# Kernel tuning notes

Measured on AMD Instinct MI355X. Metric: run time of the kernel, lower is better.

## Reference

```python
import jax, jax.numpy as jnp
import numpy as np

HEIGHT = 32
NEG = -1e30
K = 2
DEPTH_LIM = 3
BN_EPS = 1e-5


def blockwise_knn(x, k, depth_lim):
    # x: [B, C, N]. Returns global neighbor indices [B, N, k*width].
    B, C, N = x.shape
    width = N // HEIGHT
    k_eff = k * width
    xb = x.reshape(B, C, HEIGHT, width)
    win = 2 * depth_lim + 1
    offs = jnp.arange(win) - depth_lim

    def per_block(i):
        wb = i + offs
        valid = (wb >= 0) & (wb < HEIGHT)
        wbc = jnp.clip(wb, 0, HEIGHT - 1)
        cand = xb[:, :, wbc, :].reshape(B, C, win * width)   # [B,C,W]
        q = xb[:, :, i, :]                                   # [B,C,width]
        # negative squared distance: 2 q.c - |q|^2 - |c|^2 (topk largest = nearest)
        d = 2.0 * jnp.einsum('bcq,bcw->bqw', q, cand)
        d = d - jnp.sum(q * q, axis=1)[:, :, None] - jnp.sum(cand * cand, axis=1)[:, None, :]
        mask = jnp.repeat(valid, width)                      # [W]
        d = jnp.where(mask[None, None, :], d, NEG)
        _, loc = jax.lax.top_k(d, k_eff)                     # [B,width,k_eff]
        # window starts at block (i-depth_lim): local -> global point index
        return loc + (i - depth_lim) * width

    idx = jax.vmap(per_block, out_axes=1)(jnp.arange(HEIGHT))  # [B,32,width,k_eff]
    return idx.reshape(B, N, k_eff)


def get_graph_feature(x, k, depth_lim):
    B, C, N = x.shape
    idx = blockwise_knn(x, k, depth_lim)              # [B,N,K] int32
    xt = jnp.transpose(x, (0, 2, 1))                  # [B,N,C]
    feat = jax.vmap(lambda xb, ib: xb[ib])(xt, idx)   # [B,N,K,C] gather
    center = xt[:, :, None, :]
    f = jnp.concatenate([feat - center, jnp.broadcast_to(center, feat.shape)], axis=-1)
    return jnp.transpose(f, (0, 3, 1, 2))             # [B,2C,N,K]


def edge_layer(x, w, g, b, k, depth_lim):
    f = get_graph_feature(x, k, depth_lim)            # [B,2C,N,K]
    y = jnp.einsum('oc,bcnk->bonk', w, f)             # 1x1 conv, no bias
    # BatchNorm2d, train-mode batch statistics (biased variance)
    mu = jnp.mean(y, axis=(0, 2, 3), keepdims=True)
    var = jnp.mean((y - mu) ** 2, axis=(0, 2, 3), keepdims=True)
    y = (y - mu) / jnp.sqrt(var + BN_EPS) * g[None, :, None, None] + b[None, :, None, None]
    y = jnp.where(y >= 0, y, 0.2 * y)                 # LeakyReLU(0.2)
    return jnp.max(y, axis=-1)                        # max over neighbors -> [B,O,N]


def setup_inputs() -> dict:
    key = jax.random.key(0)
    ks = jax.random.split(key, 16)
    d = {}
    d['x'] = jax.random.normal(ks[0], (2, 256, 1024), jnp.float32)
    shapes = {'w0': (128, 512), 'w1': (128, 256), 'w2': (64, 256), 'w3': (64, 128)}
    for i, (name, sh) in enumerate(shapes.items()):
        d[name] = jax.random.normal(ks[1 + i], sh, jnp.float32) * (1.0 / np.sqrt(sh[1]))
        co = sh[0]
        d['g' + name[1]] = jax.random.uniform(ks[5 + i], (co,), jnp.float32, 0.5, 1.5)
        d['b' + name[1]] = jax.random.normal(ks[9 + i], (co,), jnp.float32) * 0.1
    d['w_last'] = jax.random.normal(ks[13], (384, 384), jnp.float32) * (1.0 / np.sqrt(384))
    return d


def reference(x, w0, g0, b0, w1, g1, b1, w2, g2, b2, w3, g3, b3, w_last):
    x0 = edge_layer(x, w0, g0, b0, K, DEPTH_LIM)          # [B,128,N]
    xnew = edge_layer(x0, w1, g1, b1, K, DEPTH_LIM)       # [B,128,N]
    xcon = jnp.concatenate([x0, xnew], axis=1)            # [B,256,N]
    xnew = edge_layer(xnew, w2, g2, b2, K, DEPTH_LIM)     # [B,64,N]
    xcon = jnp.concatenate([xcon, xnew], axis=1)          # [B,320,N]
    xnew = edge_layer(xnew, w3, g3, b3, K, DEPTH_LIM)     # [B,64,N]
    xcon = jnp.concatenate([xcon, xnew], axis=1)          # [B,384,N]
    return jnp.einsum('oc,bcn->bon', w_last, xcon)        # Conv1d k=1, no bias
```

## Files before the change

### kernel.cpp

```cpp
#include <hip/hip_runtime.h>
#include <math.h>

#define NPTS 1024
#define CAND 224
#define KEFF 64
#define BATCH 2
#define NEGV -1e30f
#define PLANE (BATCH * NPTS * CAND)

__global__ __launch_bounds__(256) void kprep(const float* __restrict__ w0, const float* __restrict__ w1,
                                             const float* __restrict__ w2, const float* __restrict__ w3,
                                             const float* __restrict__ wl, float* __restrict__ wt) {
    __shared__ float tA[32][33];
    __shared__ float tB[32][33];
    int id = blockIdx.x;
    int t = threadIdx.x;
    int row = t >> 5, col = t & 31;
    const float* W = w0; int Cin = 256, Co = 128; float* WtA = wt; float* WtB = wt + 32768;
    int tc = 0, to = 0; bool isWL = false;
    if (id < 32)      { int r = id;      tc = r >> 2; to = r & 3; }
    else if (id < 48) { W = w1; Cin = 128; Co = 128; WtA = wt + 65536;  WtB = wt + 81920;  int r = id - 32; tc = r >> 2; to = r & 3; }
    else if (id < 56) { W = w2; Cin = 128; Co = 64;  WtA = wt + 98304;  WtB = wt + 106496; int r = id - 48; tc = r >> 1; to = r & 1; }
    else if (id < 60) { W = w3; Cin = 64;  Co = 64;  WtA = wt + 114688; WtB = wt + 118784; int r = id - 56; tc = r >> 1; to = r & 1; }
    else { isWL = true; int r = id - 60; tc = r / 12; to = r % 12; }
    if (!isWL) {
#pragma unroll
        for (int r = 0; r < 4; ++r) {
            int o = to * 32 + row + r * 8;
            int c = tc * 32 + col;
            float va = W[(size_t)o * 2 * Cin + c];
            tA[row + r * 8][col] = va;
            tB[row + r * 8][col] = W[(size_t)o * 2 * Cin + Cin + c] - va;
        }
        __syncthreads();
#pragma unroll
        for (int r = 0; r < 4; ++r) {
            int c = tc * 32 + row + r * 8;
            int o = to * 32 + col;
            WtA[(size_t)c * Co + o] = tA[col][row + r * 8];
            WtB[(size_t)c * Co + o] = tB[col][row + r * 8];
        }
    } else {
        float* wlT = wt + 122880;
#pragma unroll
        for (int r = 0; r < 4; ++r) {
            int o = to * 32 + row + r * 8;
            int c = tc * 32 + col;
            tA[row + r * 8][col] = wl[(size_t)o * 384 + c];
        }
        __syncthreads();
#pragma unroll
        for (int r = 0; r < 4; ++r) {
            int c = tc * 32 + row + r * 8;
            int o = to * 32 + col;
            wlT[(size_t)c * 384 + o] = tA[col][row + r * 8];
        }
    }
}

struct GP {
    const float* xin; int bstride; int Cin; int Co; int nch; int applyBN;
    const float* WtA; const float* WtB;
    const float* partPrev; const float* gPrev; const float* bePrev;
    float* A; float* Bv; float* sq; float* Dp;
};

__global__ __launch_bounds__(256) void kgemm(GP p) {
    __shared__ float smem[7168];
    __shared__ float shsc[128];
    __shared__ float shsh[128];
    int t = threadIdx.x;
    if (p.applyBN && t < p.Cin) {
        const float* pp = p.partPrev;
        float s  = pp[t * 2]     + pp[(p.Cin + t) * 2];
        float s2 = pp[t * 2 + 1] + pp[(p.Cin + t) * 2 + 1];
        const float invc = 1.f / 131072.f;
        float mu = s * invc;
        float var = s2 * invc - mu * mu;
        float rs = rsqrtf(var + 1e-5f);
        float sc = p.gPrev[t] * rs;
        shsc[t] = sc;
        shsh[t] = p.bePrev[t] - mu * sc;
    }
    __syncthreads();
    int nOT = p.Co >> 6;
    int nABx = 32 * nOT * BATCH;
    if ((int)blockIdx.x < nABx) {
        int id = blockIdx.x;
        int nt = id & 31; int rest = id >> 5;
        int ot = rest % nOT; int b = rest / nOT;
        int tn2 = (t & 15) * 2, to4 = (t >> 4) * 4;
        int n0 = nt * 32, o0 = ot * 64;
        const float* xb = p.xin + (size_t)b * p.bstride + n0;
        float* Xs = smem; float* Wta = smem + 1024; float* Wtb = smem + 3200;
        float2 a2[4], b2[4], s2v;
#pragma unroll
        for (int i = 0; i < 4; ++i) { a2[i] = make_float2(0.f,0.f); b2[i] = make_float2(0.f,0.f); }
        s2v = make_float2(0.f,0.f);
        int xcc0 = t >> 5, xnn = t & 31;
        int wcc0 = t >> 6, woo = t & 63;
        for (int c0 = 0; c0 < p.Cin; c0 += 32) {
            float rx[4], ra[8], rb[8];
#pragma unroll
            for (int k = 0; k < 4; ++k)
                rx[k] = xb[(size_t)(c0 + xcc0 + k * 8) * NPTS + xnn];
#pragma unroll
            for (int k = 0; k < 8; ++k) {
                ra[k] = p.WtA[(size_t)(c0 + wcc0 + k * 4) * p.Co + o0 + woo];
                rb[k] = p.WtB[(size_t)(c0 + wcc0 + k * 4) * p.Co + o0 + woo];
            }
            if (p.applyBN) {
#pragma unroll
                for (int k = 0; k < 4; ++k) {
                    int cc = xcc0 + k * 8;
                    float y = fmaf(rx[k], shsc[c0 + cc], shsh[c0 + cc]);
                    rx[k] = y >= 0.f ? y : 0.2f * y;
                }
            }
            __syncthreads();
#pragma unroll
            for (int k = 0; k < 4; ++k)
                Xs[(xcc0 + k * 8) * 32 + xnn] = rx[k];
#pragma unroll
            for (int k = 0; k < 8; ++k) {
                Wta[(wcc0 + k * 4) * 68 + woo] = ra[k];
                Wtb[(wcc0 + k * 4) * 68 + woo] = rb[k];
            }
            __syncthreads();
#pragma unroll 8
            for (int cc = 0; cc < 32; ++cc) {
                float2 xv = *(const float2*)&Xs[cc * 32 + tn2];
                float4 wa = *(const float4*)&Wta[cc * 68 + to4];
                float4 wb = *(const float4*)&Wtb[cc * 68 + to4];
                s2v.x = fmaf(xv.x, xv.x, s2v.x);
                s2v.y = fmaf(xv.y, xv.y, s2v.y);
                float wav[4] = {wa.x, wa.y, wa.z, wa.w};
                float wbv[4] = {wb.x, wb.y, wb.z, wb.w};
#pragma unroll
                for (int i = 0; i < 4; ++i) {
                    a2[i].x = fmaf(wav[i], xv.x, a2[i].x);
                    a2[i].y = fmaf(wav[i], xv.y, a2[i].y);
                    b2[i].x = fmaf(wbv[i], xv.x, b2[i].x);
                    b2[i].y = fmaf(wbv[i], xv.y, b2[i].y);
                }
            }
        }
        int n = n0 + tn2;
        if (ot == 0 && to4 == 0)
            *(float2*)&p.sq[b * NPTS + n] = s2v;
#pragma unroll
        for (int i = 0; i < 4; ++i) {
            int o = o0 + to4 + i;
            size_t off = ((size_t)(b * p.Co + o)) * NPTS + n;
            *(float2*)&p.A[off] = a2[i];
            *(float2*)&p.Bv[off] = b2[i];
        }
    } else {
        int id2 = blockIdx.x - nABx;
        int chunk = id2 % p.nch; int rest = id2 / p.nch;
        int i = rest & 31; int b = rest >> 5;
        int c0 = chunk * 32;
        const float* xb = p.xin + (size_t)b * p.bstride;
        float* Xc = smem;
        int q = t >> 3;
        int wg = t & 7;
        float r[28];
        int rcc[28], rw[28];
#pragma unroll
        for (int k = 0; k < 28; ++k) {
            int e = t + k * 256;
            int cc = e / CAND;
            int w  = e - cc * CAND;
            rcc[k] = cc; rw[k] = w;
            int wb = i - 3 + (w >> 5);
            wb = wb < 0 ? 0 : (wb > 31 ? 31 : wb);
            r[k] = xb[(size_t)(c0 + cc) * NPTS + wb * 32 + (w & 31)];
        }
        if (p.applyBN) {
#pragma unroll
            for (int k = 0; k < 28; ++k) {
                float y = fmaf(r[k], shsc[c0 + rcc[k]], shsh[c0 + rcc[k]]);
                r[k] = y >= 0.f ? y : 0.2f * y;
            }
        }
#pragma unroll
        for (int k = 0; k < 28; ++k)
            Xc[rcc[k] * CAND + rw[k]] = r[k];
        __syncthreads();
        float acc[28];
#pragma unroll
        for (int j = 0; j < 28; ++j) acc[j] = 0.f;
        for (int cc = 0; cc < 32; ++cc) {
            float qv = Xc[cc * CAND + 96 + q];
            const float4* row = (const float4*)&Xc[cc * CAND + wg * 28];
#pragma unroll
            for (int j4 = 0; j4 < 7; ++j4) {
                float4 v = row[j4];
                acc[j4 * 4 + 0] = fmaf(qv, v.x, acc[j4 * 4 + 0]);
                acc[j4 * 4 + 1] = fmaf(qv, v.y, acc[j4 * 4 + 1]);
                acc[j4 * 4 + 2] = fmaf(qv, v.z, acc[j4 * 4 + 2]);
                acc[j4 * 4 + 3] = fmaf(qv, v.w, acc[j4 * 4 + 3]);
            }
        }
        int n = i * 32 + q;
        size_t base = (((size_t)chunk * BATCH + b) * NPTS + n) * CAND + wg * 28;
        float4* outp = (float4*)&p.Dp[base];
#pragma unroll
        for (int j4 = 0; j4 < 7; ++j4)
            outp[j4] = make_float4(acc[j4 * 4], acc[j4 * 4 + 1], acc[j4 * 4 + 2], acc[j4 * 4 + 3]);
    }
}

template<int NCH>
__global__ __launch_bounds__(256) void kselect(const float* __restrict__ Dp,
                                               const float* __restrict__ sq,
                                               int* __restrict__ idxo) {
    __shared__ ulonglong2 Dsh2[4][112];
    unsigned long long* Dsh = (unsigned long long*)Dsh2;
    int t = threadIdx.x;
    int wv = t >> 6, l = t & 63;
    int b = blockIdx.y;
    int n = blockIdx.x * 4 + wv;
    int i = n >> 5;
    float sqn = sq[b * NPTS + n];
    float pr[4][NCH];
    float sqw[4];
#pragma unroll
    for (int j = 0; j < 4; ++j) {
        int w = l + 64 * j;
        if (w < CAND) {
            size_t off = ((size_t)b * NPTS + n) * CAND + w;
#pragma unroll
            for (int ch = 0; ch < NCH; ++ch)
                pr[j][ch] = Dp[off + (size_t)ch * PLANE];
            int wb = i - 3 + (w >> 5);
            int wbc = wb < 0 ? 0 : (wb > 31 ? 31 : wb);
            sqw[j] = sq[b * NPTS + wbc * 32 + (w & 31)];
        }
    }
    unsigned long long kj[4];
#pragma unroll
    for (int j = 0; j < 4; ++j) {
        int w = l + 64 * j;
        if (w < CAND) {
            float s = 0.f;
#pragma unroll
            for (int ch = 0; ch < NCH; ++ch) s += pr[j][ch];
            int wb = i - 3 + (w >> 5);
            bool valid = (wb >= 0) && (wb < 32);
            float d = 2.f * s - sqn - sqw[j];
            d = valid ? d : NEGV;
            unsigned u = __float_as_uint(d);
            u ^= ((unsigned)((int)u >> 31)) | 0x80000000u;
            unsigned long long key = ((unsigned long long)u << 8) | (unsigned long long)(255 - w);
            kj[j] = key;
            Dsh[wv * 224 + w] = key;
        } else {
            kj[j] = 0ull;
        }
    }
    __syncthreads();
    int cnt[4] = {0, 0, 0, 0};
    const ulonglong2* row = Dsh2[wv];
#pragma unroll 2
    for (int w2 = 0; w2 < 112; w2 += 4) {
        ulonglong2 k0 = row[w2], k1 = row[w2 + 1], k2 = row[w2 + 2], k3 = row[w2 + 3];
#pragma unroll
        for (int j = 0; j < 4; ++j) {
            unsigned long long kk = kj[j];
            cnt[j] += (int)(k0.x > kk) + (int)(k0.y > kk) + (int)(k1.x > kk) + (int)(k1.y > kk)
                    + (int)(k2.x > kk) + (int)(k2.y > kk) + (int)(k3.x > kk) + (int)(k3.y > kk);
        }
    }
#pragma unroll
    for (int j = 0; j < 4; ++j) {
        int w = l + 64 * j;
        if (w < CAND && cnt[j] < KEFF)
            idxo[((size_t)b * KEFF + cnt[j]) * NPTS + n] = (i - 3) * 32 + w;
    }
}

__global__ __launch_bounds__(256) void kagg(const float* __restrict__ A, const float* __restrict__ Bv,
                                            const int* __restrict__ idx, int Co,
                                            float* __restrict__ xconM, int chOut,
                                            float* __restrict__ part) {
    __shared__ float Ash[NPTS];
    __shared__ float red[256];
    int o = blockIdx.x, b = blockIdx.y, t = threadIdx.x;
    size_t rowoff = ((size_t)(b * Co + o)) * NPTS;
    {
        float rA[4];
#pragma unroll
        for (int r = 0; r < 4; ++r) rA[r] = A[rowoff + r * 256 + t];
#pragma unroll
        for (int r = 0; r < 4; ++r) Ash[r * 256 + t] = rA[r];
    }
    __syncthreads();
    float sum = 0.f, sumsq = 0.f;
    for (int r = 0; r < 4; ++r) {
        int n = r * 256 + t;
        const int* ip = idx + (size_t)b * KEFF * NPTS + n;
        float s1 = 0.f, s2 = 0.f, mx = -3.4e38f;
#pragma unroll
        for (int kb = 0; kb < 4; ++kb) {
            int iv[16];
#pragma unroll
            for (int m = 0; m < 16; ++m)
                iv[m] = ip[(size_t)(kb * 16 + m) * NPTS];
            float av[16];
#pragma unroll
            for (int m = 0; m < 16; ++m) av[m] = Ash[iv[m]];
#pragma unroll
            for (int m = 0; m < 16; m += 4) {
                s1 += av[m] + av[m+1] + av[m+2] + av[m+3];
                s2 += av[m]*av[m] + av[m+1]*av[m+1] + av[m+2]*av[m+2] + av[m+3]*av[m+3];
                mx = fmaxf(mx, fmaxf(fmaxf(av[m], av[m+1]), fmaxf(av[m+2], av[m+3])));
            }
        }
        float bv = Bv[rowoff + n];
        xconM[((size_t)b * 384 + chOut + o) * NPTS + n] = mx + bv;
        sum   += s1 + 64.f * bv;
        sumsq += s2 + 2.f * bv * s1 + 64.f * bv * bv;
    }
    red[t] = sum; __syncthreads();
    for (int s = 128; s > 0; s >>= 1) { if (t < s) red[t] += red[t + s]; __syncthreads(); }
    if (t == 0) part[((size_t)(b * Co + o)) * 2 + 0] = red[0];
    __syncthreads();
    red[t] = sumsq; __syncthreads();
    for (int s = 128; s > 0; s >>= 1) { if (t < s) red[t] += red[t + s]; __syncthreads(); }
    if (t == 0) part[((size_t)(b * Co + o)) * 2 + 1] = red[0];
}

struct FP {
    const float* part0; const float* part1; const float* part2; const float* part3;
    const float* g0; const float* g1; const float* g2; const float* g3;
    const float* be0; const float* be1; const float* be2; const float* be3;
};

__global__ __launch_bounds__(256) void kfinal(const float* __restrict__ xconM,
                                              const float* __restrict__ wlT, FP p,
                                              float* __restrict__ out) {
    __shared__ float Xs[2048];
    __shared__ float Wl[2176];
    __shared__ float shsc[384];
    __shared__ float shsh[384];
    int t = threadIdx.x;
    for (int ch = t; ch < 384; ch += 256) {
        const float* pl; const float* gl; const float* bl; int o, Col;
        if (ch < 128)      { pl = p.part0; gl = p.g0; bl = p.be0; o = ch;       Col = 128; }
        else if (ch < 256) { pl = p.part1; gl = p.g1; bl = p.be1; o = ch - 128; Col = 128; }
        else if (ch < 320) { pl = p.part2; gl = p.g2; bl = p.be2; o = ch - 256; Col = 64;  }
        else               { pl = p.part3; gl = p.g3; bl = p.be3; o = ch - 320; Col = 64;  }
        float s  = pl[o * 2]     + pl[(Col + o) * 2];
        float s2 = pl[o * 2 + 1] + pl[(Col + o) * 2 + 1];
        const float invc = 1.f / 131072.f;
        float mu = s * invc;
        float var = s2 * invc - mu * mu;
        float rs = rsqrtf(var + 1e-5f);
        float sc = gl[o] * rs;
        shsc[ch] = sc;
        shsh[ch] = bl[o] - mu * sc;
    }
    __syncthreads();
    int tn4 = (t & 15) * 4, to4 = (t >> 4) * 4;
    int n0 = blockIdx.x * 64, o0 = blockIdx.y * 64, b = blockIdx.z;
    int cc0 = t >> 6, nn0 = t & 63;
    float4 acc[4];
#pragma unroll
    for (int i = 0; i < 4; ++i) acc[i] = make_float4(0.f,0.f,0.f,0.f);
    for (int c0 = 0; c0 < 384; c0 += 32) {
        float rx[8], rw[8];
#pragma unroll
        for (int k = 0; k < 8; ++k) {
            int cc = cc0 + k * 4;
            rx[k] = xconM[((size_t)b * 384 + c0 + cc) * NPTS + n0 + nn0];
            rw[k] = wlT[(size_t)(c0 + cc) * 384 + o0 + nn0];
        }
#pragma unroll
        for (int k = 0; k < 8; ++k) {
            int cc = cc0 + k * 4;
            float y = fmaf(rx[k], shsc[c0 + cc], shsh[c0 + cc]);
            rx[k] = y >= 0.f ? y : 0.2f * y;
        }
        __syncthreads();
#pragma unroll
        for (int k = 0; k < 8; ++k) {
            int cc = cc0 + k * 4;
            Xs[cc * 64 + nn0] = rx[k];
            Wl[cc * 68 + nn0] = rw[k];
        }
        __syncthreads();
#pragma unroll 4
        for (int cc = 0; cc < 32; ++cc) {
            float4 xv = *(const float4*)&Xs[cc * 64 + tn4];
            float4 wv = *(const float4*)&Wl[cc * 68 + to4];
            float wvv[4] = {wv.x, wv.y, wv.z, wv.w};
#pragma unroll
            for (int i = 0; i < 4; ++i) {
                acc[i].x = fmaf(wvv[i], xv.x, acc[i].x);
                acc[i].y = fmaf(wvv[i], xv.y, acc[i].y);
                acc[i].z = fmaf(wvv[i], xv.z, acc[i].z);
                acc[i].w = fmaf(wvv[i], xv.w, acc[i].w);
            }
        }
    }
#pragma unroll
    for (int i = 0; i < 4; ++i)
        *(float4*)&out[((size_t)b * 384 + o0 + to4 + i) * NPTS + n0 + tn4] = acc[i];
}

extern "C" void kernel_launch(void* const* d_in, const int* in_sizes, int n_in,
                              void* d_out, int out_size, void* d_ws, size_t ws_size,
                              hipStream_t stream) {
    const float* x  = (const float*)d_in[0];
    const float* w[4]  = {(const float*)d_in[1], (const float*)d_in[4], (const float*)d_in[7], (const float*)d_in[10]};
    const float* g[4]  = {(const float*)d_in[2], (const float*)d_in[5], (const float*)d_in[8], (const float*)d_in[11]};
    const float* be[4] = {(const float*)d_in[3], (const float*)d_in[6], (const float*)d_in[9], (const float*)d_in[12]};
    const float* wl = (const float*)d_in[13];

    float* ws    = (float*)d_ws;
    float* xconM = ws;
    float* A     = xconM + 786432;
    float* Bv    = A + 262144;
    float* sq    = Bv + 262144;
    float* Dp    = sq + 2048;
    float* part  = Dp + 3670016;
    float* wt    = part + 2048;
    int*   idx   = (int*)(wt + 270336);

    kprep<<<204, 256, 0, stream>>>(w[0], w[1], w[2], w[3], wl, wt);

    struct LC { const float* xin; int bstride; int Cin; int Co; int nch; int chOut;
                const float* wtA; const float* wtB; };
    LC L[4] = {
        { x,                  256 * 1024, 256, 128, 8, 0,   wt,          wt + 32768  },
        { xconM,              384 * 1024, 128, 128, 4, 128, wt + 65536,  wt + 81920  },
        { xconM + 128 * 1024, 384 * 1024, 128, 64,  4, 256, wt + 98304,  wt + 106496 },
        { xconM + 256 * 1024, 384 * 1024, 64,  64,  2, 320, wt + 114688, wt + 118784 },
    };

    for (int l = 0; l < 4; ++l) {
        GP gp;
        gp.xin = L[l].xin; gp.bstride = L[l].bstride; gp.Cin = L[l].Cin; gp.Co = L[l].Co;
        gp.nch = L[l].nch; gp.applyBN = (l > 0);
        gp.WtA = L[l].wtA; gp.WtB = L[l].wtB;
        gp.partPrev = (l > 0) ? part + (l - 1) * 512 : nullptr;
        gp.gPrev = (l > 0) ? g[l - 1] : nullptr;
        gp.bePrev = (l > 0) ? be[l - 1] : nullptr;
        gp.A = A; gp.Bv = Bv; gp.sq = sq; gp.Dp = Dp;
        int nAB = 32 * (L[l].Co >> 6) * BATCH;
        int nDist = L[l].nch * 32 * BATCH;
        kgemm<<<nAB + nDist, 256, 0, stream>>>(gp);
        if (L[l].nch == 8)      kselect<8><<<dim3(NPTS / 4, BATCH), 256, 0, stream>>>(Dp, sq, idx);
        else if (L[l].nch == 4) kselect<4><<<dim3(NPTS / 4, BATCH), 256, 0, stream>>>(Dp, sq, idx);
        else                    kselect<2><<<dim3(NPTS / 4, BATCH), 256, 0, stream>>>(Dp, sq, idx);
        kagg<<<dim3(L[l].Co, BATCH), 256, 0, stream>>>(A, Bv, idx, L[l].Co, xconM, L[l].chOut, part + l * 512);
    }

    FP fp;
    fp.part0 = part; fp.part1 = part + 512; fp.part2 = part + 1024; fp.part3 = part + 1536;
    fp.g0 = g[0]; fp.g1 = g[1]; fp.g2 = g[2]; fp.g3 = g[3];
    fp.be0 = be[0]; fp.be1 = be[1]; fp.be2 = be[2]; fp.be3 = be[3];
    kfinal<<<dim3(16, 6, BATCH), 256, 0, stream>>>(xconM, wt + 122880, fp, (float*)d_out);
}
```

Before: 258.7 us.

## Fuse kNN selection with neighbor aggregation and accumulate BN stats atomically

Merges the top-k selection and aggregation kernels into one kernel. Each block handles 8 query points, keeps the selected neighbor indices in shared memory, and stages the 224-wide A band per output-channel group for the gather-max. This removes the global idx buffer round trip and one launch per layer. BN partial sums are now reduced by shuffles and added with atomics into a buffer zeroed by the preceding GEMM kernel. The cost is more redundant A loads across blocks and more atomic traffic.

```diff
diff --git a/kernel.cpp b/kernel.cpp
--- a/kernel.cpp
+++ b/kernel.cpp
@@ -63,6 +63,7 @@
     const float* WtA; const float* WtB;
     const float* partPrev; const float* gPrev; const float* bePrev;
     float* A; float* Bv; float* sq; float* Dp;
+    float* partOut; int partN;
 };
 
 __global__ __launch_bounds__(256) void kgemm(GP p) {
@@ -70,6 +71,9 @@
     __shared__ float shsc[128];
     __shared__ float shsh[128];
     int t = threadIdx.x;
+    if (blockIdx.x == 0) {
+        for (int e = t; e < p.partN; e += 256) p.partOut[e] = 0.f;
+    }
     if (p.applyBN && t < p.Cin) {
         const float* pp = p.partPrev;
         float s  = pp[t * 2]     + pp[(p.Cin + t) * 2];
@@ -211,124 +215,126 @@
     }
 }
 
-template<int NCH>
-__global__ __launch_bounds__(256) void kselect(const float* __restrict__ Dp,
+template<int NCH, int CO, int CHOUT>
+__global__ __launch_bounds__(256) void kselagg(const float* __restrict__ Dp,
                                                const float* __restrict__ sq,
-                                               int* __restrict__ idxo) {
-    __shared__ ulonglong2 Dsh2[4][112];
-    unsigned long long* Dsh = (unsigned long long*)Dsh2;
+                                               const float* __restrict__ A,
+                                               const float* __restrict__ Bv,
+                                               float* __restrict__ xconM,
+                                               float* __restrict__ part) {
+    __shared__ __align__(16) float fbuf[7200];
+    __shared__ int idxsh[512];
+    unsigned long long* sKeys = (unsigned long long*)fbuf;
     int t = threadIdx.x;
-    int wv = t >> 6, l = t & 63;
+    int v = t >> 6, l = t & 63;
     int b = blockIdx.y;
-    int n = blockIdx.x * 4 + wv;
-    int i = n >> 5;
-    float sqn = sq[b * NPTS + n];
-    float pr[4][NCH];
-    float sqw[4];
-#pragma unroll
-    for (int j = 0; j < 4; ++j) {
-        int w = l + 64 * j;
-        if (w < CAND) {
-            size_t off = ((size_t)b * NPTS + n) * CAND + w;
-#pragma unroll
-            for (int ch = 0; ch < NCH; ++ch)
-                pr[j][ch] = Dp[off + (size_t)ch * PLANE];
-            int wb = i - 3 + (w >> 5);
-            int wbc = wb < 0 ? 0 : (wb > 31 ? 31 : wb);
-            sqw[j] = sq[b * NPTS + wbc * 32 + (w & 31)];
-        }
-    }
-    unsigned long long kj[4];
-#pragma unroll
-    for (int j = 0; j < 4; ++j) {
-        int w = l + 64 * j;
-        if (w < CAND) {
-            float s = 0.f;
-#pragma unroll
-            for (int ch = 0; ch < NCH; ++ch) s += pr[j][ch];
-            int wb = i - 3 + (w >> 5);
-            bool valid = (wb >= 0) && (wb < 32);
-            float d = 2.f * s - sqn - sqw[j];
-            d = valid ? d : NEGV;
-            unsigned u = __float_as_uint(d);
-            u ^= ((unsigned)((int)u >> 31)) | 0x80000000u;
-            unsigned long long key = ((unsigned long long)u << 8) | (unsigned long long)(255 - w);
-            kj[j] = key;
-            Dsh[wv * 224 + w] = key;
-        } else {
-            kj[j] = 0ull;
+    int n0 = blockIdx.x * 8;
+    int i = n0 >> 5;
+    int bandlo = (i - 3) * 32;
+
+    unsigned long long kj[2][4];
+#pragma unroll
+    for (int h = 0; h < 2; ++h) {
+        int nl = v + h * 4;
+        int n = n0 + nl;
+        float sqn = sq[b * NPTS + n];
+        float pr[4][NCH];
+        float sqw[4];
+#pragma unroll
+        for (int j = 0; j < 4; ++j) {
+            int w = l + 64 * j;
+            if (w < CAND) {
+                size_t off = ((size_t)b * NPTS + n) * CAND + w;
+#pragma unroll
+                for (int ch = 0; ch < NCH; ++ch)
+                    pr[j][ch] = Dp[off + (size_t)ch * PLANE];
+                int wb = i - 3 + (w >> 5);
+                int wbc = wb < 0 ? 0 : (wb > 31 ? 31 : wb);
+                sqw[j] = sq[b * NPTS + wbc * 32 + (w & 31)];
+            }
+        }
+#pragma unroll
+        for (int j = 0; j < 4; ++j) {
+            int w = l + 64 * j;
+            if (w < CAND) {
+                float s = 0.f;
+#pragma unroll
+                for (int ch = 0; ch < NCH; ++ch) s += pr[j][ch];
+                int wb = i - 3 + (w >> 5);
+                bool valid = (wb >= 0) && (wb < 32);
+                float d = 2.f * s - sqn - sqw[j];
+                d = valid ? d : NEGV;
+                unsigned u = __float_as_uint(d);
+                u ^= ((unsigned)((int)u >> 31)) | 0x80000000u;
+                unsigned long long key = ((unsigned long long)u << 8) | (unsigned long long)(255 - w);
+                kj[h][j] = key;
+                sKeys[nl * 224 + w] = key;
+            } else {
+                kj[h][j] = 0ull;
+            }
         }
     }
     __syncthreads();
-    int cnt[4] = {0, 0, 0, 0};
-    const ulonglong2* row = Dsh2[wv];
+#pragma unroll
+    for (int h = 0; h < 2; ++h) {
+        int nl = v + h * 4;
+        int cnt[4] = {0, 0, 0, 0};
+        const ulonglong2* row = (const ulonglong2*)(sKeys + nl * 224);
 #pragma unroll 2
-    for (int w2 = 0; w2 < 112; w2 += 4) {
-        ulonglong2 k0 = row[w2], k1 = row[w2 + 1], k2 = row[w2 + 2], k3 = row[w2 + 3];
+        for (int w2 = 0; w2 < 112; w2 += 4) {
+            ulonglong2 k0 = row[w2], k1 = row[w2 + 1], k2 = row[w2 + 2], k3 = row[w2 + 3];
+#pragma unroll
+            for (int j = 0; j < 4; ++j) {
+                unsigned long long kk = kj[h][j];
+                cnt[j] += (int)(k0.x > kk) + (int)(k0.y > kk) + (int)(k1.x > kk) + (int)(k1.y > kk)
+                        + (int)(k2.x > kk) + (int)(k2.y > kk) + (int)(k3.x > kk) + (int)(k3.y > kk);
+            }
+        }
 #pragma unroll
         for (int j = 0; j < 4; ++j) {
-            unsigned long long kk = kj[j];
-            cnt[j] += (int)(k0.x > kk) + (int)(k0.y > kk) + (int)(k1.x > kk) + (int)(k1.y > kk)
-                    + (int)(k2.x > kk) + (int)(k2.y > kk) + (int)(k3.x > kk) + (int)(k3.y > kk);
-        }
-    }
-#pragma unroll
-    for (int j = 0; j < 4; ++j) {
-        int w = l + 64 * j;
-        if (w < CAND && cnt[j] < KEFF)
-            idxo[((size_t)b * KEFF + cnt[j]) * NPTS + n] = (i - 3) * 32 + w;
-    }
-}
-
-__global__ __launch_bounds__(256) void kagg(const float* __restrict__ A, const float* __restrict__ Bv,
-                                            const int* __restrict__ idx, int Co,
-                                            float* __restrict__ xconM, int chOut,
-                                            float* __restrict__ part) {
-    __shared__ float Ash[NPTS];
-    __shared__ float red[256];
-    int o = blockIdx.x, b = blockIdx.y, t = threadIdx.x;
-    size_t rowoff = ((size_t)(b * Co + o)) * NPTS;
-    {
-        float rA[4];
-#pragma unroll
-        for (int r = 0; r < 4; ++r) rA[r] = A[rowoff + r * 256 + t];
-#pragma unroll
-        for (int r = 0; r < 4; ++r) Ash[r * 256 + t] = rA[r];
-    }
-    __syncthreads();
-    float sum = 0.f, sumsq = 0.f;
-    for (int r = 0; r < 4; ++r) {
-        int n = r * 256 + t;
-        const int* ip = idx + (size_t)b * KEFF * NPTS + n;
+            int w = l + 64 * j;
+            if (w < CAND && cnt[j] < KEFF)
+                idxsh[nl * 64 + cnt[j]] = w;
+        }
+    }
+    int oL = t >> 3;
+    int nl = t & 7;
+    int wsub = t & 7;
+    for (int og = 0; og < CO; og += 32) {
+        __syncthreads();
+#pragma unroll
+        for (int m = 0; m < 28; ++m) {
+            int w = wsub + m * 8;
+            int aidx = bandlo + w;
+            aidx = aidx < 0 ? 0 : (aidx > 1023 ? 1023 : aidx);
+            fbuf[oL * 225 + w] = A[((size_t)(b * CO + og + oL)) * NPTS + aidx];
+        }
+        __syncthreads();
+        const float* arow = &fbuf[oL * 225];
+        const int* ish = &idxsh[nl * 64];
         float s1 = 0.f, s2 = 0.f, mx = -3.4e38f;
-#pragma unroll
-        for (int kb = 0; kb < 4; ++kb) {
-            int iv[16];
-#pragma unroll
-            for (int m = 0; m < 16; ++m)
-                iv[m] = ip[(size_t)(kb * 16 + m) * NPTS];
-            float av[16];
-#pragma unroll
-            for (int m = 0; m < 16; ++m) av[m] = Ash[iv[m]];
-#pragma unroll
-            for (int m = 0; m < 16; m += 4) {
-                s1 += av[m] + av[m+1] + av[m+2] + av[m+3];
-                s2 += av[m]*av[m] + av[m+1]*av[m+1] + av[m+2]*av[m+2] + av[m+3]*av[m+3];
-                mx = fmaxf(mx, fmaxf(fmaxf(av[m], av[m+1]), fmaxf(av[m+2], av[m+3])));
-            }
-        }
-        float bv = Bv[rowoff + n];
-        xconM[((size_t)b * 384 + chOut + o) * NPTS + n] = mx + bv;
-        sum   += s1 + 64.f * bv;
-        sumsq += s2 + 2.f * bv * s1 + 64.f * bv * bv;
-    }
-    red[t] = sum; __syncthreads();
-    for (int s = 128; s > 0; s >>= 1) { if (t < s) red[t] += red[t + s]; __syncthreads(); }
-    if (t == 0) part[((size_t)(b * Co + o)) * 2 + 0] = red[0];
-    __syncthreads();
-    red[t] = sumsq; __syncthreads();
-    for (int s = 128; s > 0; s >>= 1) { if (t < s) red[t] += red[t + s]; __syncthreads(); }
-    if (t == 0) part[((size_t)(b * Co + o)) * 2 + 1] = red[0];
+#pragma unroll 8
+        for (int k = 0; k < KEFF; ++k) {
+            float a = arow[ish[k]];
+            s1 += a;
+            s2 = fmaf(a, a, s2);
+            mx = fmaxf(mx, a);
+        }
+        int n = n0 + nl;
+        float bv = Bv[((size_t)(b * CO + og + oL)) * NPTS + n];
+        xconM[((size_t)b * 384 + CHOUT + og + oL) * NPTS + n] = mx + bv;
+        float c1 = s1 + 64.f * bv;
+        float c2 = s2 + 2.f * bv * s1 + 64.f * bv * bv;
+#pragma unroll
+        for (int m = 1; m < 8; m <<= 1) {
+            c1 += __shfl_xor(c1, m);
+            c2 += __shfl_xor(c2, m);
+        }
+        if (nl == 0) {
+            atomicAdd(&part[((size_t)(b * CO + og + oL)) * 2 + 0], c1);
+            atomicAdd(&part[((size_t)(b * CO + og + oL)) * 2 + 1], c2);
+        }
+    }
 }
 
 struct FP {
@@ -426,7 +432,6 @@
     float* Dp    = sq + 2048;
     float* part  = Dp + 3670016;
     float* wt    = part + 2048;
-    int*   idx   = (int*)(wt + 270336);
 
     kprep<<<204, 256, 0, stream>>>(w[0], w[1], w[2], w[3], wl, wt);
 
@@ -448,13 +453,15 @@
         gp.gPrev = (l > 0) ? g[l - 1] : nullptr;
         gp.bePrev = (l > 0) ? be[l - 1] : nullptr;
         gp.A = A; gp.Bv = Bv; gp.sq = sq; gp.Dp = Dp;
+        gp.partOut = part + l * 512; gp.partN = L[l].Co * BATCH * 2;
         int nAB = 32 * (L[l].Co >> 6) * BATCH;
         int nDist = L[l].nch * 32 * BATCH;
         kgemm<<<nAB + nDist, 256, 0, stream>>>(gp);
-        if (L[l].nch == 8)      kselect<8><<<dim3(NPTS / 4, BATCH), 256, 0, stream>>>(Dp, sq, idx);
-        else if (L[l].nch == 4) kselect<4><<<dim3(NPTS / 4, BATCH), 256, 0, stream>>>(Dp, sq, idx);
-        else                    kselect<2><<<dim3(NPTS / 4, BATCH), 256, 0, stream>>>(Dp, sq, idx);
-        kagg<<<dim3(L[l].Co, BATCH), 256, 0, stream>>>(A, Bv, idx, L[l].Co, xconM, L[l].chOut, part + l * 512);
+        dim3 sg(NPTS / 8, BATCH);
+        if (l == 0)      kselagg<8, 128, 0  ><<<sg, 256, 0, stream>>>(Dp, sq, A, Bv, xconM, part + 0);
+        else if (l == 1) kselagg<4, 128, 128><<<sg, 256, 0, stream>>>(Dp, sq, A, Bv, xconM, part + 512);
+        else if (l == 2) kselagg<4, 64,  256><<<sg, 256, 0, stream>>>(Dp, sq, A, Bv, xconM, part + 1024);
+        else             kselagg<2, 64,  320><<<sg, 256, 0, stream>>>(Dp, sq, A, Bv, xconM, part + 1536);
     }
 
     FP fp;
```

After: 280.5 us. 1.08x slower.
